# Kernel optimization log

Hardware: AMD Instinct MI355X
Metric: run time of the kernel (lower is better)

The kernel has to match this reference:

```python
import jax, jax.numpy as jnp
import numpy as np

# Config values (from c.mean_shift / c.cuda in the original module)
EMBED_DIM = 32      # embedding_dim
BW = 2.0            # kernel_bandwidth
ETA = 0.5           # step_size
N_ITERS = 3         # nb_iterations
RES = 96            # pic_res (image is RES x RES, N = RES*RES pixels)


def setup_inputs() -> dict:
    key = jax.random.key(0)
    # Scale 0.1 keeps exp(BW * x^T x) well inside fp32 range, mimicking the
    # bounded embeddings produced by the upstream margin-loss-trained net.
    x_in = 0.1 * jax.random.normal(key, (1, EMBED_DIM, RES, RES), dtype=jnp.float32)
    return {"x_in": x_in}


def reference(x_in):
    # x_in: (1, D, RES, RES). One mean-shift step per iteration:
    #   K = exp(bw * X^T X)                      (N x N affinity)
    #   deg_j = sum_i K[i, j]                    (column degree; K is symmetric)
    #   X_new = eta * X @ (K / deg) + (1-eta) * X
    # (The original's torch.inverse(diag(deg)) is exactly 1/deg column scaling.)
    # All iterates are concatenated along dim 0, as in the torch code.
    res = x_in.shape[3]
    n = res * res
    xs = [x_in.reshape(EMBED_DIM, n)]
    for _ in range(N_ITERS):
        X = xs[-1]                                    # (D, N)
        K = jnp.exp(BW * jnp.einsum('di,dj->ij', X, X))  # (N, N)
        deg = K.sum(axis=0)                           # (N,) column sums
        xs.append(ETA * (X @ (K / deg)) + (1.0 - ETA) * X)
    # (N_ITERS+1, D, RES, RES)
    return jnp.stack(xs, axis=0).reshape(-1, EMBED_DIM, res, res)
```

## Files before the change

### kernel.cpp

```cpp
#include <hip/hip_runtime.h>
#include <hip/hip_bf16.h>


#define DIM 32
#define RESO 96
#define NPT (RESO * RESO)
#define NITER 3
#define ETA 0.5f
#define SCALE 2.88539008f

#define QB 128
#define NQB (NPT / QB)
#define KSEG 7
#define NCHUNK_TOT (NPT / 64)
#define PSTRIDE 72

typedef __bf16 bf16_t;
typedef __bf16 v8bf __attribute__((ext_vector_type(8)));
typedef float  v4f  __attribute__((ext_vector_type(4)));

__global__ void pack_kernel(const float* __restrict__ X,
                            bf16_t* __restrict__ rows,
                            bf16_t* __restrict__ cols,
                            float* __restrict__ out_copy) {
    int idx = blockIdx.x * 256 + threadIdx.x;
    if (idx >= DIM * NPT) return;
    int d = idx / NPT;
    int n = idx - d * NPT;
    float v = X[idx];
    cols[idx] = (bf16_t)v;
    rows[n * DIM + d] = (bf16_t)v;
    out_copy[idx] = v;
}

__global__ __launch_bounds__(512, 4)
void msattn_kernel(const float* __restrict__ Xcur,
                   const bf16_t* __restrict__ rows,
                   const bf16_t* __restrict__ cols,
                   float* __restrict__ part_num,
                   float* __restrict__ part_den) {
    __shared__ __align__(16) bf16_t tiles[2][4096];
    __shared__ __align__(16) bf16_t pslab[8][16 * PSTRIDE];

    const int tid  = threadIdx.x;
    const int w    = tid >> 6;
    const int lane = tid & 63;
    const int quad = lane >> 4;
    const int l16  = lane & 15;
    const int qb   = blockIdx.x;
    const int ks   = blockIdx.y;
    const int c0   = (NCHUNK_TOT * ks) / KSEG;
    const int c1   = (NCHUNK_TOT * (ks + 1)) / KSEG;
    const int q0w  = qb * QB + w * 16;

    bf16_t* p_lds = pslab[w];

    v8bf afrag;
#pragma unroll
    for (int j = 0; j < 8; ++j) {
        float v = Xcur[(quad * 8 + j) * NPT + q0w + l16];
        afrag[j] = (bf16_t)(v * SCALE);
    }

    const bf16_t* gsrc;
    int gdelta;
    if (w < 4) {
        gsrc = rows + ((size_t)c0 * 64 + 4 * l16 + w) * DIM + quad * 8;
        gdelta = 64 * DIM;
    } else {
        int r = w - 4, h = r >> 1, g = r & 1;
        gsrc = cols + (size_t)(h * 16 + l16) * NPT + c0 * 64 + g * 32 + quad * 8;
        gdelta = 64;
    }
    const int ldst = w * 512 + lane * 8;

    v4f acc0 = {0.f, 0.f, 0.f, 0.f};
    v4f acc1 = {0.f, 0.f, 0.f, 0.f};
    float den[4] = {0.f, 0.f, 0.f, 0.f};

    {
        v8bf st = *(const v8bf*)gsrc;
        gsrc += gdelta;
        *(v8bf*)&tiles[0][ldst] = st;
    }
    __syncthreads();

    for (int c = c0; c < c1; ++c) {
        const int cc = c - c0;
        const bf16_t* tb = tiles[cc & 1];
        const bool more = (c + 1 < c1);

        v8bf stn;
        if (more) { stn = *(const v8bf*)gsrc; gsrc += gdelta; }

        v4f s[4];
#pragma unroll
        for (int t = 0; t < 4; ++t) {
            v8bf b = *(const v8bf*)&tb[t * 512 + lane * 8];
            s[t] = __builtin_amdgcn_mfma_f32_16x16x32_bf16(afrag, b,
                                                           (v4f){0.f, 0.f, 0.f, 0.f}, 0, 0, 0);
        }

#pragma unroll
        for (int r = 0; r < 4; ++r) {
            union { bf16_t h[4]; unsigned long long u; } pk;
#pragma unroll
            for (int t = 0; t < 4; ++t) {
                float wv = __builtin_amdgcn_exp2f(s[t][r]);
                den[r] += wv;
                pk.h[t] = (bf16_t)wv;
            }
            *(unsigned long long*)&p_lds[(quad * 4 + r) * PSTRIDE + 4 * l16] = pk.u;
        }

        v8bf a20 = *(const v8bf*)&p_lds[l16 * PSTRIDE + quad * 8];
        v8bf a21 = *(const v8bf*)&p_lds[l16 * PSTRIDE + 32 + quad * 8];
        v8bf b00 = *(const v8bf*)&tb[2048 + 0 * 512 + lane * 8];
        v8bf b01 = *(const v8bf*)&tb[2048 + 1 * 512 + lane * 8];
        v8bf b10 = *(const v8bf*)&tb[2048 + 2 * 512 + lane * 8];
        v8bf b11 = *(const v8bf*)&tb[2048 + 3 * 512 + lane * 8];
        acc0 = __builtin_amdgcn_mfma_f32_16x16x32_bf16(a20, b00, acc0, 0, 0, 0);
        acc1 = __builtin_amdgcn_mfma_f32_16x16x32_bf16(a20, b10, acc1, 0, 0, 0);
        acc0 = __builtin_amdgcn_mfma_f32_16x16x32_bf16(a21, b01, acc0, 0, 0, 0);
        acc1 = __builtin_amdgcn_mfma_f32_16x16x32_bf16(a21, b11, acc1, 0, 0, 0);

        if (more) *(v8bf*)&tiles[(cc + 1) & 1][ldst] = stn;
        __syncthreads();
    }

#pragma unroll
    for (int m = 1; m < 16; m <<= 1) {
#pragma unroll
        for (int r = 0; r < 4; ++r) den[r] += __shfl_xor(den[r], m);
    }
    float* pn = part_num + (size_t)ks * NPT * DIM;
#pragma unroll
    for (int r = 0; r < 4; ++r) {
        int gq = q0w + quad * 4 + r;
        pn[(size_t)gq * DIM + l16]      = acc0[r];
        pn[(size_t)gq * DIM + 16 + l16] = acc1[r];
    }
    if (l16 == 0) {
#pragma unroll
        for (int r = 0; r < 4; ++r)
            part_den[ks * NPT + q0w + quad * 4 + r] = den[r];
    }
}

__global__ __launch_bounds__(256, 4)
void reduce_kernel(const float* __restrict__ part_num,
                   const float* __restrict__ part_den,
                   const float* __restrict__ Xcur,
                   float* __restrict__ Xnext,
                   bf16_t* __restrict__ rows_out,
                   bf16_t* __restrict__ cols_out) {
    __shared__ float tnum[32][33];
    __shared__ float txn[32][33];
    __shared__ float tden[32];

    const int tid = threadIdx.x;
    const int q0  = blockIdx.x * 32;

#pragma unroll
    for (int j = 0; j < 4; ++j) {
        int idx = tid + j * 256;
        int qq = idx >> 5, d = idx & 31;
        float s = 0.f;
#pragma unroll
        for (int ss = 0; ss < KSEG; ++ss)
            s += part_num[((size_t)ss * NPT + q0 + qq) * DIM + d];
        tnum[qq][d] = s;
    }
    if (tid < 32) {
        float s = 0.f;
#pragma unroll
        for (int ss = 0; ss < KSEG; ++ss)
            s += part_den[ss * NPT + q0 + tid];
        tden[tid] = s;
    }
    __syncthreads();

#pragma unroll
    for (int j = 0; j < 4; ++j) {
        int idx = tid + j * 256;
        int d = idx >> 5, qq = idx & 31;
        float num = tnum[qq][d];
        float dn  = tden[qq];
        float xo  = Xcur[d * NPT + q0 + qq];
        float xn  = ETA * num / dn + (1.0f - ETA) * xo;
        Xnext[d * NPT + q0 + qq] = xn;
        cols_out[(size_t)d * NPT + q0 + qq] = (bf16_t)xn;
        txn[qq][d] = xn;
    }
    __syncthreads();

#pragma unroll
    for (int j = 0; j < 4; ++j) {
        int idx = tid + j * 256;
        int qq = idx >> 5, d = idx & 31;
        rows_out[(size_t)(q0 + qq) * DIM + d] = (bf16_t)txn[qq][d];
    }
}

extern "C" void kernel_launch(void* const* d_in, const int* in_sizes, int n_in,
                              void* d_out, int out_size, void* d_ws, size_t ws_size,
                              hipStream_t stream) {
    const float* x_in = (const float*)d_in[0];
    float* out = (float*)d_out;

    const size_t DN = (size_t)DIM * NPT;
    bf16_t* rows0 = (bf16_t*)d_ws;
    bf16_t* cols0 = rows0 + DN;
    bf16_t* rows1 = cols0 + DN;
    bf16_t* cols1 = rows1 + DN;
    float* part_num = (float*)(cols1 + DN);
    float* part_den = part_num + (size_t)KSEG * NPT * DIM;

    const int pack_blocks = (DIM * NPT + 255) / 256;
    pack_kernel<<<pack_blocks, 256, 0, stream>>>(x_in, rows0, cols0, out);

    for (int it = 0; it < NITER; ++it) {
        const float* Xcur = (it == 0) ? x_in : out + (size_t)it * DN;
        bf16_t* rin  = (it & 1) ? rows1 : rows0;
        bf16_t* cin  = (it & 1) ? cols1 : cols0;
        bf16_t* rout = (it & 1) ? rows0 : rows1;
        bf16_t* cout = (it & 1) ? cols0 : cols1;
        msattn_kernel<<<dim3(NQB, KSEG), 512, 0, stream>>>(Xcur, rin, cin,
                                                           part_num, part_den);
        reduce_kernel<<<NPT / 32, 256, 0, stream>>>(part_num, part_den, Xcur,
                                                    out + (size_t)(it + 1) * DN,
                                                    rout, cout);
    }
}
```

Measured before the change: 137.3 us.

## Give each wave 32 query rows and double the key-split segments

Each block now runs 4 waves of 256 threads instead of 8 waves, and each wave handles two 16-row query tiles. The shared K/V tile loaded from LDS is reused across both tiles, and each wave issues two global loads per chunk for the cooperative tile fill. The key dimension is split into 14 segments instead of 7, so the grid stays large enough to fill the GPU. The trade-off is higher register pressure per wave and twice as many partial-sum writes that the reduce kernel must read back.

```diff
diff --git a/kernel.cpp b/kernel.cpp
--- a/kernel.cpp
+++ b/kernel.cpp
@@ -10,8 +10,9 @@
 #define SCALE 2.88539008f
 
 #define QB 128
+#define NWAVE 4
 #define NQB (NPT / QB)
-#define KSEG 7
+#define KSEG 14
 #define NCHUNK_TOT (NPT / 64)
 #define PSTRIDE 72
 
@@ -33,14 +34,14 @@
     out_copy[idx] = v;
 }
 
-__global__ __launch_bounds__(512, 4)
+__global__ __launch_bounds__(256, 4)
 void msattn_kernel(const float* __restrict__ Xcur,
                    const bf16_t* __restrict__ rows,
                    const bf16_t* __restrict__ cols,
                    float* __restrict__ part_num,
                    float* __restrict__ part_den) {
     __shared__ __align__(16) bf16_t tiles[2][4096];
-    __shared__ __align__(16) bf16_t pslab[8][16 * PSTRIDE];
+    __shared__ __align__(16) bf16_t pslab[NWAVE][32 * PSTRIDE];
 
     const int tid  = threadIdx.x;
     const int w    = tid >> 6;
@@ -51,37 +52,47 @@
     const int ks   = blockIdx.y;
     const int c0   = (NCHUNK_TOT * ks) / KSEG;
     const int c1   = (NCHUNK_TOT * (ks + 1)) / KSEG;
-    const int q0w  = qb * QB + w * 16;
+    const int q0w  = qb * QB + w * 32;
 
     bf16_t* p_lds = pslab[w];
 
-    v8bf afrag;
+    v8bf afrag0, afrag1;
 #pragma unroll
     for (int j = 0; j < 8; ++j) {
-        float v = Xcur[(quad * 8 + j) * NPT + q0w + l16];
-        afrag[j] = (bf16_t)(v * SCALE);
-    }
-
-    const bf16_t* gsrc;
-    int gdelta;
-    if (w < 4) {
-        gsrc = rows + ((size_t)c0 * 64 + 4 * l16 + w) * DIM + quad * 8;
-        gdelta = 64 * DIM;
-    } else {
-        int r = w - 4, h = r >> 1, g = r & 1;
-        gsrc = cols + (size_t)(h * 16 + l16) * NPT + c0 * 64 + g * 32 + quad * 8;
-        gdelta = 64;
-    }
-    const int ldst = w * 512 + lane * 8;
-
-    v4f acc0 = {0.f, 0.f, 0.f, 0.f};
-    v4f acc1 = {0.f, 0.f, 0.f, 0.f};
-    float den[4] = {0.f, 0.f, 0.f, 0.f};
-
-    {
-        v8bf st = *(const v8bf*)gsrc;
-        gsrc += gdelta;
-        *(v8bf*)&tiles[0][ldst] = st;
+        const float* src = Xcur + (quad * 8 + j) * NPT + q0w + l16;
+        afrag0[j] = (bf16_t)(src[0] * SCALE);
+        afrag1[j] = (bf16_t)(src[16] * SCALE);
+    }
+
+    const bf16_t* gsrc[2];
+    int gdelta[2], ldst[2];
+#pragma unroll
+    for (int i = 0; i < 2; ++i) {
+        int p = 2 * w + i;
+        if (p < 4) {
+            gsrc[i] = rows + ((size_t)c0 * 64 + 4 * l16 + p) * DIM + quad * 8;
+            gdelta[i] = 64 * DIM;
+            ldst[i] = p * 512 + lane * 8;
+        } else {
+            int r = p - 4, h = r >> 1, g = r & 1;
+            gsrc[i] = cols + (size_t)(h * 16 + l16) * NPT + c0 * 64 + g * 32 + quad * 8;
+            gdelta[i] = 64;
+            ldst[i] = 2048 + r * 512 + lane * 8;
+        }
+    }
+
+    v4f acc00 = {0.f, 0.f, 0.f, 0.f};
+    v4f acc01 = {0.f, 0.f, 0.f, 0.f};
+    v4f acc10 = {0.f, 0.f, 0.f, 0.f};
+    v4f acc11 = {0.f, 0.f, 0.f, 0.f};
+    float den0[4] = {0.f, 0.f, 0.f, 0.f};
+    float den1[4] = {0.f, 0.f, 0.f, 0.f};
+
+#pragma unroll
+    for (int i = 0; i < 2; ++i) {
+        v8bf st = *(const v8bf*)gsrc[i];
+        gsrc[i] += gdelta[i];
+        *(v8bf*)&tiles[0][ldst[i]] = st;
     }
     __syncthreads();
 
@@ -90,60 +101,88 @@
         const bf16_t* tb = tiles[cc & 1];
         const bool more = (c + 1 < c1);
 
-        v8bf stn;
-        if (more) { stn = *(const v8bf*)gsrc; gsrc += gdelta; }
-
-        v4f s[4];
+        v8bf stn0, stn1;
+        if (more) {
+            stn0 = *(const v8bf*)gsrc[0]; gsrc[0] += gdelta[0];
+            stn1 = *(const v8bf*)gsrc[1]; gsrc[1] += gdelta[1];
+        }
+
+        v4f s0[4], s1[4];
 #pragma unroll
         for (int t = 0; t < 4; ++t) {
             v8bf b = *(const v8bf*)&tb[t * 512 + lane * 8];
-            s[t] = __builtin_amdgcn_mfma_f32_16x16x32_bf16(afrag, b,
-                                                           (v4f){0.f, 0.f, 0.f, 0.f}, 0, 0, 0);
+            s0[t] = __builtin_amdgcn_mfma_f32_16x16x32_bf16(afrag0, b,
+                                                            (v4f){0.f, 0.f, 0.f, 0.f}, 0, 0, 0);
+            s1[t] = __builtin_amdgcn_mfma_f32_16x16x32_bf16(afrag1, b,
+                                                            (v4f){0.f, 0.f, 0.f, 0.f}, 0, 0, 0);
         }
 
 #pragma unroll
         for (int r = 0; r < 4; ++r) {
-            union { bf16_t h[4]; unsigned long long u; } pk;
+            union { bf16_t h[4]; unsigned long long u; } pk0, pk1;
 #pragma unroll
             for (int t = 0; t < 4; ++t) {
-                float wv = __builtin_amdgcn_exp2f(s[t][r]);
-                den[r] += wv;
-                pk.h[t] = (bf16_t)wv;
+                float w0 = __builtin_amdgcn_exp2f(s0[t][r]);
+                float w1 = __builtin_amdgcn_exp2f(s1[t][r]);
+                den0[r] += w0; den1[r] += w1;
+                pk0.h[t] = (bf16_t)w0; pk1.h[t] = (bf16_t)w1;
             }
-            *(unsigned long long*)&p_lds[(quad * 4 + r) * PSTRIDE + 4 * l16] = pk.u;
-        }
-
-        v8bf a20 = *(const v8bf*)&p_lds[l16 * PSTRIDE + quad * 8];
-        v8bf a21 = *(const v8bf*)&p_lds[l16 * PSTRIDE + 32 + quad * 8];
+            *(unsigned long long*)&p_lds[(quad * 4 + r) * PSTRIDE + 4 * l16] = pk0.u;
+            *(unsigned long long*)&p_lds[(16 + quad * 4 + r) * PSTRIDE + 4 * l16] = pk1.u;
+        }
+
         v8bf b00 = *(const v8bf*)&tb[2048 + 0 * 512 + lane * 8];
         v8bf b01 = *(const v8bf*)&tb[2048 + 1 * 512 + lane * 8];
         v8bf b10 = *(const v8bf*)&tb[2048 + 2 * 512 + lane * 8];
         v8bf b11 = *(const v8bf*)&tb[2048 + 3 * 512 + lane * 8];
-        acc0 = __builtin_amdgcn_mfma_f32_16x16x32_bf16(a20, b00, acc0, 0, 0, 0);
-        acc1 = __builtin_amdgcn_mfma_f32_16x16x32_bf16(a20, b10, acc1, 0, 0, 0);
-        acc0 = __builtin_amdgcn_mfma_f32_16x16x32_bf16(a21, b01, acc0, 0, 0, 0);
-        acc1 = __builtin_amdgcn_mfma_f32_16x16x32_bf16(a21, b11, acc1, 0, 0, 0);
-
-        if (more) *(v8bf*)&tiles[(cc + 1) & 1][ldst] = stn;
+        {
+            v8bf a20 = *(const v8bf*)&p_lds[l16 * PSTRIDE + quad * 8];
+            v8bf a21 = *(const v8bf*)&p_lds[l16 * PSTRIDE + 32 + quad * 8];
+            acc00 = __builtin_amdgcn_mfma_f32_16x16x32_bf16(a20, b00, acc00, 0, 0, 0);
+            acc01 = __builtin_amdgcn_mfma_f32_16x16x32_bf16(a20, b10, acc01, 0, 0, 0);
+            acc00 = __builtin_amdgcn_mfma_f32_16x16x32_bf16(a21, b01, acc00, 0, 0, 0);
+            acc01 = __builtin_amdgcn_mfma_f32_16x16x32_bf16(a21, b11, acc01, 0, 0, 0);
+        }
+        {
+            v8bf a20 = *(const v8bf*)&p_lds[(16 + l16) * PSTRIDE + quad * 8];
+            v8bf a21 = *(const v8bf*)&p_lds[(16 + l16) * PSTRIDE + 32 + quad * 8];
+            acc10 = __builtin_amdgcn_mfma_f32_16x16x32_bf16(a20, b00, acc10, 0, 0, 0);
+            acc11 = __builtin_amdgcn_mfma_f32_16x16x32_bf16(a20, b10, acc11, 0, 0, 0);
+            acc10 = __builtin_amdgcn_mfma_f32_16x16x32_bf16(a21, b01, acc10, 0, 0, 0);
+            acc11 = __builtin_amdgcn_mfma_f32_16x16x32_bf16(a21, b11, acc11, 0, 0, 0);
+        }
+
+        if (more) {
+            *(v8bf*)&tiles[(cc + 1) & 1][ldst[0]] = stn0;
+            *(v8bf*)&tiles[(cc + 1) & 1][ldst[1]] = stn1;
+        }
         __syncthreads();
     }
 
 #pragma unroll
     for (int m = 1; m < 16; m <<= 1) {
 #pragma unroll
-        for (int r = 0; r < 4; ++r) den[r] += __shfl_xor(den[r], m);
+        for (int r = 0; r < 4; ++r) {
+            den0[r] += __shfl_xor(den0[r], m);
+            den1[r] += __shfl_xor(den1[r], m);
+        }
     }
     float* pn = part_num + (size_t)ks * NPT * DIM;
 #pragma unroll
     for (int r = 0; r < 4; ++r) {
-        int gq = q0w + quad * 4 + r;
-        pn[(size_t)gq * DIM + l16]      = acc0[r];
-        pn[(size_t)gq * DIM + 16 + l16] = acc1[r];
+        int gq0 = q0w + quad * 4 + r;
+        int gq1 = gq0 + 16;
+        pn[(size_t)gq0 * DIM + l16]      = acc00[r];
+        pn[(size_t)gq0 * DIM + 16 + l16] = acc01[r];
+        pn[(size_t)gq1 * DIM + l16]      = acc10[r];
+        pn[(size_t)gq1 * DIM + 16 + l16] = acc11[r];
     }
     if (l16 == 0) {
 #pragma unroll
-        for (int r = 0; r < 4; ++r)
-            part_den[ks * NPT + q0w + quad * 4 + r] = den[r];
+        for (int r = 0; r < 4; ++r) {
+            part_den[ks * NPT + q0w + quad * 4 + r]      = den0[r];
+            part_den[ks * NPT + q0w + 16 + quad * 4 + r] = den1[r];
+        }
     }
 }
 
@@ -225,7 +264,7 @@
         bf16_t* cin  = (it & 1) ? cols1 : cols0;
         bf16_t* rout = (it & 1) ? rows0 : rows1;
         bf16_t* cout = (it & 1) ? cols0 : cols1;
-        msattn_kernel<<<dim3(NQB, KSEG), 512, 0, stream>>>(Xcur, rin, cin,
+        msattn_kernel<<<dim3(NQB, KSEG), 256, 0, stream>>>(Xcur, rin, cin,
                                                            part_num, part_den);
         reduce_kernel<<<NPT / 32, 256, 0, stream>>>(part_num, part_den, Xcur,
                                                     out + (size_t)(it + 1) * DN,
```

Result: slower. 147.7 us (+7.6%).

## Fuse split-K reduction into attention kernel via last-block atomic counter

Applied to the files above, without the earlier changes.

Removes the separate reduce kernel: each query block's K-segment blocks bump an atomic counter, and the last one to arrive sums the partial numerators and denominators and writes the next iterate plus its bf16 row and column copies. The denominator is now computed on the matrix cores with an MFMA against a ones vector, replacing the scalar exp accumulation and shuffle reduction. KSEG drops from 7 to 4, which shrinks the grid and the partial-sum traffic but gives fewer blocks to fill the GPU. The changes add a per-launch memset and fence/atomic overhead, and the final reduction is serialized on the last-arriving block.

```diff
diff --git a/kernel.cpp b/kernel.cpp
--- a/kernel.cpp
+++ b/kernel.cpp
@@ -10,10 +10,13 @@
 #define SCALE 2.88539008f
 
 #define QB 128
+#define NWAVE 8
 #define NQB (NPT / QB)
-#define KSEG 7
+#define KSEG 4
 #define NCHUNK_TOT (NPT / 64)
+#define CSEG (NCHUNK_TOT / KSEG)
 #define PSTRIDE 72
+#define DN (DIM * NPT)
 
 typedef __bf16 bf16_t;
 typedef __bf16 v8bf __attribute__((ext_vector_type(8)));
@@ -24,7 +27,7 @@
                             bf16_t* __restrict__ cols,
                             float* __restrict__ out_copy) {
     int idx = blockIdx.x * 256 + threadIdx.x;
-    if (idx >= DIM * NPT) return;
+    if (idx >= DN) return;
     int d = idx / NPT;
     int n = idx - d * NPT;
     float v = X[idx];
@@ -33,14 +36,19 @@
     out_copy[idx] = v;
 }
 
-__global__ __launch_bounds__(512, 4)
+__global__ __launch_bounds__(512, 2)
 void msattn_kernel(const float* __restrict__ Xcur,
                    const bf16_t* __restrict__ rows,
                    const bf16_t* __restrict__ cols,
                    float* __restrict__ part_num,
-                   float* __restrict__ part_den) {
+                   float* __restrict__ part_den,
+                   float* __restrict__ Xnext,
+                   bf16_t* __restrict__ rows_out,
+                   bf16_t* __restrict__ cols_out,
+                   unsigned int* __restrict__ ctr) {
     __shared__ __align__(16) bf16_t tiles[2][4096];
-    __shared__ __align__(16) bf16_t pslab[8][16 * PSTRIDE];
+    __shared__ __align__(16) bf16_t pslab[NWAVE][16 * PSTRIDE];
+    __shared__ unsigned int lastflag;
 
     const int tid  = threadIdx.x;
     const int w    = tid >> 6;
@@ -49,8 +57,8 @@
     const int l16  = lane & 15;
     const int qb   = blockIdx.x;
     const int ks   = blockIdx.y;
-    const int c0   = (NCHUNK_TOT * ks) / KSEG;
-    const int c1   = (NCHUNK_TOT * (ks + 1)) / KSEG;
+    const int c0   = ks * CSEG;
+    const int c1   = c0 + CSEG;
     const int q0w  = qb * QB + w * 16;
 
     bf16_t* p_lds = pslab[w];
@@ -62,21 +70,26 @@
         afrag[j] = (bf16_t)(v * SCALE);
     }
 
+    v8bf ones;
+#pragma unroll
+    for (int j = 0; j < 8; ++j) ones[j] = (bf16_t)1.0f;
+
     const bf16_t* gsrc;
-    int gdelta;
+    int gdelta, ldst;
     if (w < 4) {
         gsrc = rows + ((size_t)c0 * 64 + 4 * l16 + w) * DIM + quad * 8;
         gdelta = 64 * DIM;
+        ldst = w * 512 + lane * 8;
     } else {
         int r = w - 4, h = r >> 1, g = r & 1;
         gsrc = cols + (size_t)(h * 16 + l16) * NPT + c0 * 64 + g * 32 + quad * 8;
         gdelta = 64;
-    }
-    const int ldst = w * 512 + lane * 8;
+        ldst = 2048 + r * 512 + lane * 8;
+    }
 
     v4f acc0 = {0.f, 0.f, 0.f, 0.f};
     v4f acc1 = {0.f, 0.f, 0.f, 0.f};
-    float den[4] = {0.f, 0.f, 0.f, 0.f};
+    v4f dden = {0.f, 0.f, 0.f, 0.f};
 
     {
         v8bf st = *(const v8bf*)gsrc;
@@ -105,11 +118,8 @@
         for (int r = 0; r < 4; ++r) {
             union { bf16_t h[4]; unsigned long long u; } pk;
 #pragma unroll
-            for (int t = 0; t < 4; ++t) {
-                float wv = __builtin_amdgcn_exp2f(s[t][r]);
-                den[r] += wv;
-                pk.h[t] = (bf16_t)wv;
-            }
+            for (int t = 0; t < 4; ++t)
+                pk.h[t] = (bf16_t)__builtin_amdgcn_exp2f(s[t][r]);
             *(unsigned long long*)&p_lds[(quad * 4 + r) * PSTRIDE + 4 * l16] = pk.u;
         }
 
@@ -123,17 +133,14 @@
         acc1 = __builtin_amdgcn_mfma_f32_16x16x32_bf16(a20, b10, acc1, 0, 0, 0);
         acc0 = __builtin_amdgcn_mfma_f32_16x16x32_bf16(a21, b01, acc0, 0, 0, 0);
         acc1 = __builtin_amdgcn_mfma_f32_16x16x32_bf16(a21, b11, acc1, 0, 0, 0);
+        dden = __builtin_amdgcn_mfma_f32_16x16x32_bf16(a20, ones, dden, 0, 0, 0);
+        dden = __builtin_amdgcn_mfma_f32_16x16x32_bf16(a21, ones, dden, 0, 0, 0);
 
         if (more) *(v8bf*)&tiles[(cc + 1) & 1][ldst] = stn;
         __syncthreads();
     }
 
-#pragma unroll
-    for (int m = 1; m < 16; m <<= 1) {
-#pragma unroll
-        for (int r = 0; r < 4; ++r) den[r] += __shfl_xor(den[r], m);
-    }
-    float* pn = part_num + (size_t)ks * NPT * DIM;
+    float* pn = part_num + (size_t)ks * DN;
 #pragma unroll
     for (int r = 0; r < 4; ++r) {
         int gq = q0w + quad * 4 + r;
@@ -143,62 +150,44 @@
     if (l16 == 0) {
 #pragma unroll
         for (int r = 0; r < 4; ++r)
-            part_den[ks * NPT + q0w + quad * 4 + r] = den[r];
-    }
-}
-
-__global__ __launch_bounds__(256, 4)
-void reduce_kernel(const float* __restrict__ part_num,
-                   const float* __restrict__ part_den,
-                   const float* __restrict__ Xcur,
-                   float* __restrict__ Xnext,
-                   bf16_t* __restrict__ rows_out,
-                   bf16_t* __restrict__ cols_out) {
-    __shared__ float tnum[32][33];
-    __shared__ float txn[32][33];
-    __shared__ float tden[32];
-
-    const int tid = threadIdx.x;
-    const int q0  = blockIdx.x * 32;
-
-#pragma unroll
-    for (int j = 0; j < 4; ++j) {
-        int idx = tid + j * 256;
-        int qq = idx >> 5, d = idx & 31;
+            part_den[ks * NPT + q0w + quad * 4 + r] = dden[r];
+    }
+
+    __threadfence();
+    __syncthreads();
+    if (tid == 0) {
+        lastflag = __hip_atomic_fetch_add(&ctr[qb], 1u,
+                                          __ATOMIC_ACQ_REL,
+                                          __HIP_MEMORY_SCOPE_AGENT);
+    }
+    __syncthreads();
+    if (lastflag != KSEG - 1) return;
+
+    const int q0b = qb * QB;
+    float* sden = (float*)pslab;
+    if (tid < QB) {
         float s = 0.f;
 #pragma unroll
         for (int ss = 0; ss < KSEG; ++ss)
-            s += part_num[((size_t)ss * NPT + q0 + qq) * DIM + d];
-        tnum[qq][d] = s;
-    }
-    if (tid < 32) {
+            s += part_den[ss * NPT + q0b + tid];
+        sden[tid] = 1.0f / s;
+    }
+    __syncthreads();
+#pragma unroll
+    for (int j = 0; j < (QB * DIM) / 512; ++j) {
+        int idx = tid + j * 512;
+        int d = idx >> 7;
+        int q = idx & 127;
+        int gq = q0b + q;
         float s = 0.f;
 #pragma unroll
         for (int ss = 0; ss < KSEG; ++ss)
-            s += part_den[ss * NPT + q0 + tid];
-        tden[tid] = s;
-    }
-    __syncthreads();
-
-#pragma unroll
-    for (int j = 0; j < 4; ++j) {
-        int idx = tid + j * 256;
-        int d = idx >> 5, qq = idx & 31;
-        float num = tnum[qq][d];
-        float dn  = tden[qq];
-        float xo  = Xcur[d * NPT + q0 + qq];
-        float xn  = ETA * num / dn + (1.0f - ETA) * xo;
-        Xnext[d * NPT + q0 + qq] = xn;
-        cols_out[(size_t)d * NPT + q0 + qq] = (bf16_t)xn;
-        txn[qq][d] = xn;
-    }
-    __syncthreads();
-
-#pragma unroll
-    for (int j = 0; j < 4; ++j) {
-        int idx = tid + j * 256;
-        int qq = idx >> 5, d = idx & 31;
-        rows_out[(size_t)(q0 + qq) * DIM + d] = (bf16_t)txn[qq][d];
+            s += part_num[(size_t)ss * DN + (size_t)gq * DIM + d];
+        float xo = Xcur[d * NPT + gq];
+        float xn = ETA * s * sden[q] + (1.0f - ETA) * xo;
+        Xnext[d * NPT + gq] = xn;
+        cols_out[(size_t)d * NPT + gq] = (bf16_t)xn;
+        rows_out[(size_t)gq * DIM + d] = (bf16_t)xn;
     }
 }
 
@@ -208,15 +197,18 @@
     const float* x_in = (const float*)d_in[0];
     float* out = (float*)d_out;
 
-    const size_t DN = (size_t)DIM * NPT;
     bf16_t* rows0 = (bf16_t*)d_ws;
-    bf16_t* cols0 = rows0 + DN;
-    bf16_t* rows1 = cols0 + DN;
-    bf16_t* cols1 = rows1 + DN;
-    float* part_num = (float*)(cols1 + DN);
-    float* part_den = part_num + (size_t)KSEG * NPT * DIM;
-
-    const int pack_blocks = (DIM * NPT + 255) / 256;
+    bf16_t* cols0 = rows0 + (size_t)DN;
+    bf16_t* rows1 = cols0 + (size_t)DN;
+    bf16_t* cols1 = rows1 + (size_t)DN;
+    float* part_num = (float*)(cols1 + (size_t)DN);
+    float* part_den = part_num + (size_t)KSEG * DN;
+    size_t ctr_off = (((size_t)(part_den + KSEG * NPT) - (size_t)d_ws) + 255) & ~(size_t)255;
+    unsigned int* ctr = (unsigned int*)((char*)d_ws + ctr_off);
+
+    hipMemsetAsync(ctr, 0, NITER * NQB * sizeof(unsigned int), stream);
+
+    const int pack_blocks = (DN + 255) / 256;
     pack_kernel<<<pack_blocks, 256, 0, stream>>>(x_in, rows0, cols0, out);
 
     for (int it = 0; it < NITER; ++it) {
@@ -225,10 +217,8 @@
         bf16_t* cin  = (it & 1) ? cols1 : cols0;
         bf16_t* rout = (it & 1) ? rows0 : rows1;
         bf16_t* cout = (it & 1) ? cols0 : cols1;
-        msattn_kernel<<<dim3(NQB, KSEG), 512, 0, stream>>>(Xcur, rin, cin,
-                                                           part_num, part_den);
-        reduce_kernel<<<NPT / 32, 256, 0, stream>>>(part_num, part_den, Xcur,
-                                                    out + (size_t)(it + 1) * DN,
-                                                    rout, cout);
+        msattn_kernel<<<dim3(NQB, KSEG), 512, 0, stream>>>(
+            Xcur, rin, cin, part_num, part_den,
+            out + (size_t)(it + 1) * DN, rout, cout, ctr + it * NQB);
     }
 }
```

Result: slower. 372.3 us (+171.1%).
